# Performance work log

Hardware: AMD Instinct MI355X
Metric: run time of the kernel (lower is better)

Reference implementation:

```python
import jax, jax.numpy as jnp
import jax.lax as lax
import numpy as np

B, T, I, HS = 32, 2048, 256, 256
H = HS // 2  # per-direction hidden (hidden_size even -> fwd/bwd both H)


def setup_inputs() -> dict:
    key = jax.random.key(0)
    ks = jax.random.split(key, 10)
    s = 1.0 / np.sqrt(H)
    u = lambda k, shape: jax.random.uniform(k, shape, jnp.float32, -s, s)
    x = jax.random.normal(ks[0], (B, T, I), jnp.float32)
    lengths = jax.random.randint(ks[1], (B,), 1, T + 1)
    return {
        "x": x,
        "lengths": lengths,
        "Wf_ih": u(ks[2], (4 * H, I)), "Wf_hh": u(ks[3], (4 * H, H)),
        "bf_ih": u(ks[4], (4 * H,)), "bf_hh": u(ks[5], (4 * H,)),
        "Wb_ih": u(ks[6], (4 * H, I)), "Wb_hh": u(ks[7], (4 * H, H)),
        "bb_ih": u(ks[8], (4 * H,)), "bb_hh": u(ks[9], (4 * H,)),
    }


def _lstm_scan(x_seq, W_ih, W_hh, b_ih, b_hh):
    # x_seq: [B, T, I] -> hidden states per step [B, T, H]
    xg = jnp.einsum('bti,gi->btg', x_seq, W_ih) + b_ih  # input gates precomputed

    def step(carry, xg_t):
        h, c = carry
        gates = xg_t + h @ W_hh.T + b_hh  # [B, 4H]
        i, f, g, o = jnp.split(gates, 4, axis=-1)
        c = jax.nn.sigmoid(f) * c + jax.nn.sigmoid(i) * jnp.tanh(g)
        h = jax.nn.sigmoid(o) * jnp.tanh(c)
        return (h, c), h

    b, hdim = x_seq.shape[0], W_hh.shape[1]
    init = (jnp.zeros((b, hdim), x_seq.dtype), jnp.zeros((b, hdim), x_seq.dtype))
    _, hs = lax.scan(step, init, jnp.swapaxes(xg, 0, 1))  # [T, B, H]
    return jnp.swapaxes(hs, 0, 1)


def _flip_padded_seq(x, lengths):
    # reverse the first `length` steps of each sequence, keep padding in place
    t = jnp.arange(x.shape[1])[None, :]
    L = lengths[:, None]
    idx = jnp.where(t < L, L - 1 - t, t)  # [B, T]
    return jnp.take_along_axis(x, idx[:, :, None], axis=1)


def reference(x, lengths, Wf_ih, Wf_hh, bf_ih, bf_hh, Wb_ih, Wb_hh, bb_ih, bb_hh):
    fwd = _lstm_scan(x, Wf_ih, Wf_hh, bf_ih, bf_hh)
    x_rev = _flip_padded_seq(x, lengths)
    bwd = _lstm_scan(x_rev, Wb_ih, Wb_hh, bb_ih, bb_hh)
    return jnp.concatenate([fwd, bwd], axis=-1)  # [B, T, hidden_size]
```

## Files before the change

### kernel.cpp

```cpp
#include <hip/hip_runtime.h>
#include <hip/hip_fp16.h>

#define B_  32
#define T_  2048
#define I_  256
#define H_  128

typedef _Float16 f16;
typedef _Float16 f16x2 __attribute__((ext_vector_type(2)));
typedef _Float16 f16x4 __attribute__((ext_vector_type(4)));
typedef _Float16 f16x8 __attribute__((ext_vector_type(8)));
typedef float    f32x4 __attribute__((ext_vector_type(4)));

#if __has_builtin(__builtin_amdgcn_fdot2)
#define FDOT2(a, b, c) __builtin_amdgcn_fdot2((a), (b), (c), false)
#else
static __device__ __forceinline__ float FDOT2(f16x2 a, f16x2 b, float c) {
  return c + (float)a[0] * (float)b[0] + (float)a[1] * (float)b[1];
}
#endif

static __device__ __forceinline__ f16x2 asf16x2(unsigned u) {
  return __builtin_bit_cast(f16x2, u);
}

static __device__ __forceinline__ float fast_sig(float x) {
  float e = __builtin_amdgcn_exp2f(-1.44269504089f * x);
  return __builtin_amdgcn_rcpf(1.0f + e);
}
static __device__ __forceinline__ float fast_tanh(float x) {
  float e = __builtin_amdgcn_exp2f(-2.88539008178f * x);
  return 2.0f * __builtin_amdgcn_rcpf(1.0f + e) - 1.0f;
}

#define BARRIER_LDS()                                   \
  __builtin_amdgcn_sched_barrier(0);                    \
  asm volatile("s_waitcnt lgkmcnt(0)" ::: "memory");    \
  __builtin_amdgcn_s_barrier();                         \
  __builtin_amdgcn_sched_barrier(0)

#define MFMA16(a, b, c) __builtin_amdgcn_mfma_f32_16x16x32_f16((a), (b), (c), 0, 0, 0)

__global__ __launch_bounds__(256) void xg_gemm(
    const float* __restrict__ x,
    const float* __restrict__ Wf, const float* __restrict__ Wb,
    const float* __restrict__ bf_ih, const float* __restrict__ bf_hh,
    const float* __restrict__ bb_ih, const float* __restrict__ bb_hh,
    f16* __restrict__ xg)
{
  __shared__ f16 xs[128][136];
  __shared__ f16 wt[128][136];

  const int tid = threadIdx.x;
  const int m0  = blockIdx.y * 128;
  const int n0  = blockIdx.x * 128;

  const float* Wsrc; const float* bih; const float* bhh; int nb;
  if (n0 < 512) { Wsrc = Wf; bih = bf_ih; bhh = bf_hh; nb = n0; }
  else          { Wsrc = Wb; bih = bb_ih; bhh = bb_hh; nb = n0 - 512; }

  const int w  = tid >> 6;
  const int l  = tid & 63;
  const int lr = l & 15;
  const int lk = (l >> 4) * 8;

  f32x4 acc[2][8] = {};

  #pragma unroll
  for (int kh = 0; kh < 2; ++kh) {
    #pragma unroll
    for (int it = 0; it < 16; ++it) {
      int idx = it * 256 + tid;
      int row = idx >> 5, c4 = idx & 31;
      float4 v = *(const float4*)&x[(size_t)(m0 + row) * I_ + kh * 128 + c4 * 4];
      f16x4 h4 = { (f16)v.x, (f16)v.y, (f16)v.z, (f16)v.w };
      *(f16x4*)&xs[row][c4 * 4] = h4;
    }
    #pragma unroll
    for (int it = 0; it < 16; ++it) {
      int idx = it * 256 + tid;
      int row = idx >> 5, c4 = idx & 31;
      float4 v = *(const float4*)&Wsrc[(size_t)(nb + row) * I_ + kh * 128 + c4 * 4];
      f16x4 h4 = { (f16)v.x, (f16)v.y, (f16)v.z, (f16)v.w };
      *(f16x4*)&wt[row][c4 * 4] = h4;
    }
    __syncthreads();

    #pragma unroll
    for (int ks = 0; ks < 4; ++ks) {
      int kk = ks * 32 + lk;
      f16x8 a0 = *(const f16x8*)&xs[w * 32 + lr][kk];
      f16x8 a1 = *(const f16x8*)&xs[w * 32 + 16 + lr][kk];
      #pragma unroll
      for (int nt = 0; nt < 8; ++nt) {
        f16x8 bf = *(const f16x8*)&wt[nt * 16 + lr][kk];
        acc[0][nt] = MFMA16(a0, bf, acc[0][nt]);
        acc[1][nt] = MFMA16(a1, bf, acc[1][nt]);
      }
    }
    __syncthreads();
  }

  #pragma unroll
  for (int mt = 0; mt < 2; ++mt) {
    #pragma unroll
    for (int nt = 0; nt < 8; ++nt) {
      int nloc = nt * 16 + lr;
      float bias = bih[nb + nloc] + bhh[nb + nloc];
      #pragma unroll
      for (int r = 0; r < 4; ++r) {
        int m = m0 + w * 32 + mt * 16 + (l >> 4) * 4 + r;
        xg[(size_t)m * 1024 + n0 + nloc] = (f16)(acc[mt][nt][r] + bias);
      }
    }
  }
}

__global__ __launch_bounds__(256, 1) void birnn_rec(
    const f16* __restrict__ xg,
    const float* __restrict__ Wfhh, const float* __restrict__ Wbhh,
    const int* __restrict__ lengths,
    float* __restrict__ out)
{
  const int tid  = threadIdx.x;
  const int w    = tid >> 6;
  const int l    = tid & 63;
  const int role = l >> 5;
  const int ul   = w * 32 + (l & 31);
  const int dir  = blockIdx.x >> 5;
  const int b    = blockIdx.x & 31;
  const float* Whh = dir ? Wbhh : Wfhh;
  const int L    = lengths[b];

  const int rowA = role ? (128 + ul) : ul;
  const int rowB = rowA + 256;

  unsigned w0[64], w1[64];
  #pragma unroll
  for (int j = 0; j < 32; ++j) {
    float4 v = *(const float4*)&Whh[(size_t)rowA * H_ + j * 4];
    w0[2 * j]     = __builtin_bit_cast(unsigned, (f16x2){ (f16)v.x, (f16)v.y });
    w0[2 * j + 1] = __builtin_bit_cast(unsigned, (f16x2){ (f16)v.z, (f16)v.w });
    float4 u = *(const float4*)&Whh[(size_t)rowB * H_ + j * 4];
    w1[2 * j]     = __builtin_bit_cast(unsigned, (f16x2){ (f16)u.x, (f16)u.y });
    w1[2 * j + 1] = __builtin_bit_cast(unsigned, (f16x2){ (f16)u.z, (f16)u.w });
  }

  __shared__ __align__(16) f16 hbuf[2][128];
  if (tid < 128) hbuf[0][tid] = (f16)0.0f;
  float c = 0.0f;
  __syncthreads();

  auto rowof = [&](int t) -> size_t {
    int it = t;
    if (dir) it = (t < L) ? (L - 1 - t) : t;
    return ((size_t)(b * T_ + it)) * 1024 + (size_t)dir * 512;
  };

  f16 pa0, pa1, pb0, pb1;
  { size_t r = rowof(0); pa0 = xg[r + rowA]; pa1 = xg[r + rowB]; }
  { size_t r = rowof(1); pb0 = xg[r + rowA]; pb1 = xg[r + rowB]; }

  const float bscale = role ? 1.0f : 2.0f;
  const float bmul   = role ? 1.0f : 2.0f;
  const float badd   = role ? 0.0f : -1.0f;

#define STEP(t, P0, P1, RB, WB)                                              \
  {                                                                          \
    float aA[4] = { (float)(P0), 0.f, 0.f, 0.f };                            \
    float aB[4] = { (float)(P1), 0.f, 0.f, 0.f };                            \
    if ((t) + 2 < T_) {                                                      \
      size_t r2 = rowof((t) + 2);                                            \
      (P0) = xg[r2 + rowA];                                                  \
      (P1) = xg[r2 + rowB];                                                  \
    }                                                                        \
    _Pragma("unroll")                                                        \
    for (int j4 = 0; j4 < 16; ++j4) {                                        \
      uint4 hv = *(const uint4*)&hbuf[RB][j4 * 8];                           \
      aA[0] = FDOT2(asf16x2(hv.x), asf16x2(w0[j4 * 4 + 0]), aA[0]);          \
      aB[0] = FDOT2(asf16x2(hv.x), asf16x2(w1[j4 * 4 + 0]), aB[0]);          \
      aA[1] = FDOT2(asf16x2(hv.y), asf16x2(w0[j4 * 4 + 1]), aA[1]);          \
      aB[1] = FDOT2(asf16x2(hv.y), asf16x2(w1[j4 * 4 + 1]), aB[1]);          \
      aA[2] = FDOT2(asf16x2(hv.z), asf16x2(w0[j4 * 4 + 2]), aA[2]);          \
      aB[2] = FDOT2(asf16x2(hv.z), asf16x2(w1[j4 * 4 + 2]), aB[2]);          \
      aA[3] = FDOT2(asf16x2(hv.w), asf16x2(w0[j4 * 4 + 3]), aA[3]);          \
      aB[3] = FDOT2(asf16x2(hv.w), asf16x2(w1[j4 * 4 + 3]), aB[3]);          \
    }                                                                        \
    float sumA = (aA[0] + aA[1]) + (aA[2] + aA[3]);                          \
    float sumB = (aB[0] + aB[1]) + (aB[2] + aB[3]);                          \
      \
    float sA = fast_sig(sumA);                                               \
    float sB = fast_sig(bscale * sumB) * bmul + badd;                        \
    float pA = __shfl_xor(sA, 32, 64);                                       \
    float pB = __shfl_xor(sB, 32, 64);                                       \
    float is_ = role ? pA : sA;                                              \
    float gt_ = role ? pB : sB;                                              \
    float fs_ = role ? sA : pA;                                              \
    float os_ = role ? sB : pB;                                              \
    c = fs_ * c + is_ * gt_;                                                 \
    float hval = os_ * fast_tanh(c);                                         \
    if (!role) {                                                             \
      hbuf[WB][ul] = (f16)hval;                                              \
      out[((size_t)(b * T_ + (t))) * 256 + dir * 128 + ul] = hval;           \
    }                                                                        \
    BARRIER_LDS();                                                           \
  }

  for (int tt = 0; tt < T_; tt += 2) {
    STEP(tt,     pa0, pa1, 0, 1);
    STEP(tt + 1, pb0, pb1, 1, 0);
  }
#undef STEP
}

extern "C" void kernel_launch(void* const* d_in, const int* in_sizes, int n_in,
                              void* d_out, int out_size, void* d_ws, size_t ws_size,
                              hipStream_t stream) {
  const float* x      = (const float*)d_in[0];
  const int*   lengths= (const int*)  d_in[1];
  const float* Wf_ih  = (const float*)d_in[2];
  const float* Wf_hh  = (const float*)d_in[3];
  const float* bf_ih  = (const float*)d_in[4];
  const float* bf_hh  = (const float*)d_in[5];
  const float* Wb_ih  = (const float*)d_in[6];
  const float* Wb_hh  = (const float*)d_in[7];
  const float* bb_ih  = (const float*)d_in[8];
  const float* bb_hh  = (const float*)d_in[9];
  float* out = (float*)d_out;
  f16*   xg  = (f16*)d_ws;

  (void)in_sizes; (void)n_in; (void)out_size; (void)ws_size;

  xg_gemm<<<dim3(8, 512), 256, 0, stream>>>(x, Wf_ih, Wb_ih,
                                            bf_ih, bf_hh, bb_ih, bb_hh, xg);
  birnn_rec<<<dim3(64), 256, 0, stream>>>(xg, Wf_hh, Wb_hh, lengths, out);
}
```

Measured before the change: 1.347 ms.

## Split recurrent matvec over 1024 threads with gate-interleaved xg layout

The recurrent kernel now runs 1024 threads per block. Each thread holds a 16-element K-slice of all four gate rows for one hidden unit and reduces partial dot products with cross-lane shuffles. The xg GEMM output is reordered so the four gates of a unit sit next to each other, which lets each step's input-gate values be fetched with a single 8-byte load and prefetched 4 steps ahead. The goal is a shorter serial dependency chain per timestep, since each thread does 32 dot2 ops instead of 128. The cost is three shuffle-reduction rounds per step and block-wide barriers over 16 waves instead of 4.

```diff
diff --git a/kernel.cpp b/kernel.cpp
--- a/kernel.cpp
+++ b/kernel.cpp
@@ -55,9 +55,9 @@
   const int m0  = blockIdx.y * 128;
   const int n0  = blockIdx.x * 128;
 
-  const float* Wsrc; const float* bih; const float* bhh; int nb;
-  if (n0 < 512) { Wsrc = Wf; bih = bf_ih; bhh = bf_hh; nb = n0; }
-  else          { Wsrc = Wb; bih = bb_ih; bhh = bb_hh; nb = n0 - 512; }
+  const float* Wsrc; const float* bih; const float* bhh; int nb; size_t dbase;
+  if (n0 < 512) { Wsrc = Wf; bih = bf_ih; bhh = bf_hh; nb = n0;       dbase = 0; }
+  else          { Wsrc = Wb; bih = bb_ih; bhh = bb_hh; nb = n0 - 512; dbase = 512; }
 
   const int w  = tid >> 6;
   const int l  = tid & 63;
@@ -106,44 +106,45 @@
     #pragma unroll
     for (int nt = 0; nt < 8; ++nt) {
       int nloc = nt * 16 + lr;
-      float bias = bih[nb + nloc] + bhh[nb + nloc];
+      int grow = nb + nloc;
+      int gate = grow >> 7, unit = grow & 127;
+      size_t col = dbase + (size_t)unit * 4 + gate;
+      float bias = bih[grow] + bhh[grow];
       #pragma unroll
       for (int r = 0; r < 4; ++r) {
         int m = m0 + w * 32 + mt * 16 + (l >> 4) * 4 + r;
-        xg[(size_t)m * 1024 + n0 + nloc] = (f16)(acc[mt][nt][r] + bias);
+        xg[(size_t)m * 1024 + col] = (f16)(acc[mt][nt][r] + bias);
       }
     }
   }
 }
 
-__global__ __launch_bounds__(256, 1) void birnn_rec(
+__global__ __launch_bounds__(1024, 4) void birnn_rec(
     const f16* __restrict__ xg,
     const float* __restrict__ Wfhh, const float* __restrict__ Wbhh,
     const int* __restrict__ lengths,
     float* __restrict__ out)
 {
-  const int tid  = threadIdx.x;
-  const int w    = tid >> 6;
-  const int l    = tid & 63;
-  const int role = l >> 5;
-  const int ul   = w * 32 + (l & 31);
-  const int dir  = blockIdx.x >> 5;
-  const int b    = blockIdx.x & 31;
+  const int tid = threadIdx.x;
+  const int w   = tid >> 6;
+  const int l   = tid & 63;
+  const int ks  = (l & 3) | ((l >> 5) << 2);
+  const int u   = w * 8 + ((l >> 2) & 7);
+  const int dir = blockIdx.x >> 5;
+  const int b   = blockIdx.x & 31;
   const float* Whh = dir ? Wbhh : Wfhh;
-  const int L    = lengths[b];
-
-  const int rowA = role ? (128 + ul) : ul;
-  const int rowB = rowA + 256;
-
-  unsigned w0[64], w1[64];
+  const int L   = lengths[b];
+
+  unsigned wrg[4][8];
   #pragma unroll
-  for (int j = 0; j < 32; ++j) {
-    float4 v = *(const float4*)&Whh[(size_t)rowA * H_ + j * 4];
-    w0[2 * j]     = __builtin_bit_cast(unsigned, (f16x2){ (f16)v.x, (f16)v.y });
-    w0[2 * j + 1] = __builtin_bit_cast(unsigned, (f16x2){ (f16)v.z, (f16)v.w });
-    float4 u = *(const float4*)&Whh[(size_t)rowB * H_ + j * 4];
-    w1[2 * j]     = __builtin_bit_cast(unsigned, (f16x2){ (f16)u.x, (f16)u.y });
-    w1[2 * j + 1] = __builtin_bit_cast(unsigned, (f16x2){ (f16)u.z, (f16)u.w });
+  for (int g = 0; g < 4; ++g) {
+    const float* src = &Whh[(size_t)(g * 128 + u) * H_ + ks * 16];
+    #pragma unroll
+    for (int j = 0; j < 4; ++j) {
+      float4 v = *(const float4*)&src[j * 4];
+      wrg[g][2 * j]     = __builtin_bit_cast(unsigned, (f16x2){ (f16)v.x, (f16)v.y });
+      wrg[g][2 * j + 1] = __builtin_bit_cast(unsigned, (f16x2){ (f16)v.z, (f16)v.w });
+    }
   }
 
   __shared__ __align__(16) f16 hbuf[2][128];
@@ -154,61 +155,80 @@
   auto rowof = [&](int t) -> size_t {
     int it = t;
     if (dir) it = (t < L) ? (L - 1 - t) : t;
-    return ((size_t)(b * T_ + it)) * 1024 + (size_t)dir * 512;
+    return ((size_t)(b * T_ + it)) * 1024 + (size_t)dir * 512 + (size_t)u * 4;
   };
 
-  f16 pa0, pa1, pb0, pb1;
-  { size_t r = rowof(0); pa0 = xg[r + rowA]; pa1 = xg[r + rowB]; }
-  { size_t r = rowof(1); pb0 = xg[r + rowA]; pb1 = xg[r + rowB]; }
-
-  const float bscale = role ? 1.0f : 2.0f;
-  const float bmul   = role ? 1.0f : 2.0f;
-  const float badd   = role ? 0.0f : -1.0f;
-
-#define STEP(t, P0, P1, RB, WB)                                              \
+  uint2 pa = *(const uint2*)(xg + rowof(0));
+  uint2 pb = *(const uint2*)(xg + rowof(1));
+  uint2 pc = *(const uint2*)(xg + rowof(2));
+  uint2 pd = *(const uint2*)(xg + rowof(3));
+
+  const bool writer = (ks == 0);
+
+#define STEP(t, P, RB, WB)                                                   \
   {                                                                          \
-    float aA[4] = { (float)(P0), 0.f, 0.f, 0.f };                            \
-    float aB[4] = { (float)(P1), 0.f, 0.f, 0.f };                            \
-    if ((t) + 2 < T_) {                                                      \
-      size_t r2 = rowof((t) + 2);                                            \
-      (P0) = xg[r2 + rowA];                                                  \
-      (P1) = xg[r2 + rowB];                                                  \
-    }                                                                        \
-    _Pragma("unroll")                                                        \
-    for (int j4 = 0; j4 < 16; ++j4) {                                        \
-      uint4 hv = *(const uint4*)&hbuf[RB][j4 * 8];                           \
-      aA[0] = FDOT2(asf16x2(hv.x), asf16x2(w0[j4 * 4 + 0]), aA[0]);          \
-      aB[0] = FDOT2(asf16x2(hv.x), asf16x2(w1[j4 * 4 + 0]), aB[0]);          \
-      aA[1] = FDOT2(asf16x2(hv.y), asf16x2(w0[j4 * 4 + 1]), aA[1]);          \
-      aB[1] = FDOT2(asf16x2(hv.y), asf16x2(w1[j4 * 4 + 1]), aB[1]);          \
-      aA[2] = FDOT2(asf16x2(hv.z), asf16x2(w0[j4 * 4 + 2]), aA[2]);          \
-      aB[2] = FDOT2(asf16x2(hv.z), asf16x2(w1[j4 * 4 + 2]), aB[2]);          \
-      aA[3] = FDOT2(asf16x2(hv.w), asf16x2(w0[j4 * 4 + 3]), aA[3]);          \
-      aB[3] = FDOT2(asf16x2(hv.w), asf16x2(w1[j4 * 4 + 3]), aB[3]);          \
-    }                                                                        \
-    float sumA = (aA[0] + aA[1]) + (aA[2] + aA[3]);                          \
-    float sumB = (aB[0] + aB[1]) + (aB[2] + aB[3]);                          \
-      \
-    float sA = fast_sig(sumA);                                               \
-    float sB = fast_sig(bscale * sumB) * bmul + badd;                        \
-    float pA = __shfl_xor(sA, 32, 64);                                       \
-    float pB = __shfl_xor(sB, 32, 64);                                       \
-    float is_ = role ? pA : sA;                                              \
-    float gt_ = role ? pB : sB;                                              \
-    float fs_ = role ? sA : pA;                                              \
-    float os_ = role ? sB : pB;                                              \
-    c = fs_ * c + is_ * gt_;                                                 \
-    float hval = os_ * fast_tanh(c);                                         \
-    if (!role) {                                                             \
-      hbuf[WB][ul] = (f16)hval;                                              \
-      out[((size_t)(b * T_ + (t))) * 256 + dir * 128 + ul] = hval;           \
+    f16x4 xv = __builtin_bit_cast(f16x4, P);                                 \
+    if ((t) + 4 < T_) P = *(const uint2*)(xg + rowof((t) + 4));              \
+    uint4 hva = *(const uint4*)&hbuf[RB][ks * 16];                           \
+    uint4 hvb = *(const uint4*)&hbuf[RB][ks * 16 + 8];                       \
+    float ai = 0.f, af = 0.f, ag = 0.f, ao = 0.f;                            \
+    ai = FDOT2(asf16x2(hva.x), asf16x2(wrg[0][0]), ai);                      \
+    af = FDOT2(asf16x2(hva.x), asf16x2(wrg[1][0]), af);                      \
+    ag = FDOT2(asf16x2(hva.x), asf16x2(wrg[2][0]), ag);                      \
+    ao = FDOT2(asf16x2(hva.x), asf16x2(wrg[3][0]), ao);                      \
+    ai = FDOT2(asf16x2(hva.y), asf16x2(wrg[0][1]), ai);                      \
+    af = FDOT2(asf16x2(hva.y), asf16x2(wrg[1][1]), af);                      \
+    ag = FDOT2(asf16x2(hva.y), asf16x2(wrg[2][1]), ag);                      \
+    ao = FDOT2(asf16x2(hva.y), asf16x2(wrg[3][1]), ao);                      \
+    ai = FDOT2(asf16x2(hva.z), asf16x2(wrg[0][2]), ai);                      \
+    af = FDOT2(asf16x2(hva.z), asf16x2(wrg[1][2]), af);                      \
+    ag = FDOT2(asf16x2(hva.z), asf16x2(wrg[2][2]), ag);                      \
+    ao = FDOT2(asf16x2(hva.z), asf16x2(wrg[3][2]), ao);                      \
+    ai = FDOT2(asf16x2(hva.w), asf16x2(wrg[0][3]), ai);                      \
+    af = FDOT2(asf16x2(hva.w), asf16x2(wrg[1][3]), af);                      \
+    ag = FDOT2(asf16x2(hva.w), asf16x2(wrg[2][3]), ag);                      \
+    ao = FDOT2(asf16x2(hva.w), asf16x2(wrg[3][3]), ao);                      \
+    ai = FDOT2(asf16x2(hvb.x), asf16x2(wrg[0][4]), ai);                      \
+    af = FDOT2(asf16x2(hvb.x), asf16x2(wrg[1][4]), af);                      \
+    ag = FDOT2(asf16x2(hvb.x), asf16x2(wrg[2][4]), ag);                      \
+    ao = FDOT2(asf16x2(hvb.x), asf16x2(wrg[3][4]), ao);                      \
+    ai = FDOT2(asf16x2(hvb.y), asf16x2(wrg[0][5]), ai);                      \
+    af = FDOT2(asf16x2(hvb.y), asf16x2(wrg[1][5]), af);                      \
+    ag = FDOT2(asf16x2(hvb.y), asf16x2(wrg[2][5]), ag);                      \
+    ao = FDOT2(asf16x2(hvb.y), asf16x2(wrg[3][5]), ao);                      \
+    ai = FDOT2(asf16x2(hvb.z), asf16x2(wrg[0][6]), ai);                      \
+    af = FDOT2(asf16x2(hvb.z), asf16x2(wrg[1][6]), af);                      \
+    ag = FDOT2(asf16x2(hvb.z), asf16x2(wrg[2][6]), ag);                      \
+    ao = FDOT2(asf16x2(hvb.z), asf16x2(wrg[3][6]), ao);                      \
+    ai = FDOT2(asf16x2(hvb.w), asf16x2(wrg[0][7]), ai);                      \
+    af = FDOT2(asf16x2(hvb.w), asf16x2(wrg[1][7]), af);                      \
+    ag = FDOT2(asf16x2(hvb.w), asf16x2(wrg[2][7]), ag);                      \
+    ao = FDOT2(asf16x2(hvb.w), asf16x2(wrg[3][7]), ao);                      \
+             \
+    ai += __shfl_xor(ai, 1, 64);  af += __shfl_xor(af, 1, 64);               \
+    ag += __shfl_xor(ag, 1, 64);  ao += __shfl_xor(ao, 1, 64);               \
+    ai += __shfl_xor(ai, 2, 64);  af += __shfl_xor(af, 2, 64);               \
+    ag += __shfl_xor(ag, 2, 64);  ao += __shfl_xor(ao, 2, 64);               \
+    ai += __shfl_xor(ai, 32, 64); af += __shfl_xor(af, 32, 64);              \
+    ag += __shfl_xor(ag, 32, 64); ao += __shfl_xor(ao, 32, 64);              \
+    float is = fast_sig(ai + (float)xv[0]);                                  \
+    float fs = fast_sig(af + (float)xv[1]);                                  \
+    float gt = fast_tanh(ag + (float)xv[2]);                                 \
+    float os = fast_sig(ao + (float)xv[3]);                                  \
+    c = fs * c + is * gt;                                                    \
+    float hval = os * fast_tanh(c);                                          \
+    if (writer) {                                                            \
+      hbuf[WB][u] = (f16)hval;                                               \
+      out[((size_t)(b * T_ + (t))) * 256 + dir * 128 + u] = hval;            \
     }                                                                        \
     BARRIER_LDS();                                                           \
   }
 
-  for (int tt = 0; tt < T_; tt += 2) {
-    STEP(tt,     pa0, pa1, 0, 1);
-    STEP(tt + 1, pb0, pb1, 1, 0);
+  for (int tt = 0; tt < T_; tt += 4) {
+    STEP(tt,     pa, 0, 1);
+    STEP(tt + 1, pb, 1, 0);
+    STEP(tt + 2, pc, 0, 1);
+    STEP(tt + 3, pd, 1, 0);
   }
 #undef STEP
 }
@@ -233,5 +253,5 @@
 
   xg_gemm<<<dim3(8, 512), 256, 0, stream>>>(x, Wf_ih, Wb_ih,
                                             bf_ih, bf_hh, bb_ih, bb_hh, xg);
-  birnn_rec<<<dim3(64), 256, 0, stream>>>(xg, Wf_hh, Wb_hh, lengths, out);
-}
+  birnn_rec<<<dim3(64), 1024, 0, stream>>>(xg, Wf_hh, Wb_hh, lengths, out);
+}
```

After: 1.952 ms. 44.9% more time.
